# Performance work log

Measured on AMD Instinct MI355X. Metric: run time of the kernel, lower is better.

## Reference

```python
import jax, jax.numpy as jnp
import numpy as np

NEG_INIT = -1.0e9  # matches torch.full(..., -1000000000.0)

def setup_inputs() -> dict:
    key = jax.random.key(0)
    ks = jax.random.split(key, 12)
    N, B, F, C = 4_000_000, 16384, 3, 4
    flat_muons = jax.random.normal(ks[0], (N, F), dtype=jnp.float32)
    batch_index = jnp.sort(jax.random.randint(ks[1], (N,), 0, B))
    conditions = jax.random.normal(ks[2], (B, C), dtype=jnp.float32)
    def lin(k, fin, fout):
        k1, k2 = jax.random.split(k)
        bound = 1.0 / np.sqrt(fin)
        W = jax.random.uniform(k1, (fin, fout), jnp.float32, -bound, bound)
        b = jax.random.uniform(k2, (fout,), jnp.float32, -bound, bound)
        return W, b
    W1, b1 = lin(ks[3], F + C, 64)
    W2, b2 = lin(ks[4], 64, 128)
    W3, b3 = lin(ks[5], 128 + C, 128)
    W4, b4 = lin(ks[6], 128, 1)
    return {"flat_muons": flat_muons, "batch_index": batch_index,
            "conditions": conditions, "batch_size": B,
            "W1": W1, "b1": b1, "W2": W2, "b2": b2,
            "W3": W3, "b3": b3, "W4": W4, "b4": b4}

def reference(flat_muons, batch_index, conditions, batch_size,
              W1, b1, W2, b2, W3, b3, W4, b4):
    lrelu = lambda x: jax.nn.leaky_relu(x, 0.2)
    flat_cond = conditions[batch_index]                       # [N, C] gather
    point_in = jnp.concatenate([flat_muons, flat_cond], axis=1)
    h = lrelu(point_in @ W1 + b1)                             # [N, 64]
    point_feats = lrelu(h @ W2 + b2)                          # [N, 128]
    # segmented amax with -1e9 baseline (scatter_reduce_ amax semantics)
    global_feats = jnp.full((batch_size, 128), NEG_INIT, dtype=point_feats.dtype)
    global_feats = global_feats.at[batch_index].max(point_feats)
    decision_in = jnp.concatenate([global_feats, conditions], axis=1)
    score = lrelu(decision_in @ W3 + b3) @ W4 + b4            # [B, 1]
    return score
```

## Files before the change

### kernel.cpp

```cpp
#include <hip/hip_runtime.h>

typedef float f32x4 __attribute__((ext_vector_type(4)));
typedef float f32x16 __attribute__((ext_vector_type(16)));
typedef _Float16 half8 __attribute__((ext_vector_type(8)));
typedef _Float16 half2v __attribute__((ext_vector_type(2)));
typedef unsigned u32x4 __attribute__((ext_vector_type(4)));

__device__ __forceinline__ unsigned f2mono(float f) {
  unsigned u = __float_as_uint(f);
  return (u & 0x80000000u) ? ~u : (u | 0x80000000u);
}
__device__ __forceinline__ float mono2f(unsigned u) {
  return (u & 0x80000000u) ? __uint_as_float(u & 0x7fffffffu) : __uint_as_float(~u);
}
__device__ __forceinline__ float lrelu(float x) { return fmaxf(x, 0.2f * x); }
__device__ __forceinline__ unsigned pkrtz(float a, float b) {
  return __builtin_bit_cast(unsigned, __builtin_amdgcn_cvt_pkrtz(a, b));
}
__device__ __forceinline__ unsigned lrelu_pk(float a, float b) {
  const half2v v = __builtin_bit_cast(half2v, pkrtz(a, b));
  const half2v s = v * (half2v){(_Float16)0.2f, (_Float16)0.2f};
  return __builtin_bit_cast(unsigned, __builtin_elementwise_max(v, s));
}
__device__ __forceinline__ half8 ash8(u32x4 u) { return __builtin_bit_cast(half8, u); }
__device__ __forceinline__ float max16(const f32x16& a) {
  const float m1 = fmaxf(fmaxf(a[0], a[1]), a[2]);
  const float m2 = fmaxf(fmaxf(a[3], a[4]), a[5]);
  const float m3 = fmaxf(fmaxf(a[6], a[7]), a[8]);
  const float m4 = fmaxf(fmaxf(a[9], a[10]), a[11]);
  const float m5 = fmaxf(fmaxf(a[12], a[13]), a[14]);
  return fmaxf(fmaxf(fmaxf(m1, m2), m3), fmaxf(fmaxf(m4, m5), a[15]));
}
__device__ __forceinline__ void plswap(unsigned& x, unsigned& y) {
  asm volatile("v_permlane32_swap_b32 %0, %1" : "+v"(x), "+v"(y));
}
__device__ __forceinline__ float xhalf_max(float m) {
  unsigned a = __float_as_uint(m), b = a;
  plswap(a, b);
  return fmaxf(__uint_as_float(a), __uint_as_float(b));
}

__global__ void sc_init(unsigned* __restrict__ gf, int total4) {
  int i = blockIdx.x * blockDim.x + threadIdx.x;
  if (i < total4) {
    unsigned m = f2mono(-1.0e9f);
    ((uint4*)gf)[i] = make_uint4(m, m, m, m);
  }
}

__global__ __launch_bounds__(256, 2) void sc_main(
    const float* __restrict__ muons, const int* __restrict__ bidx,
    const float* __restrict__ cond, const float* __restrict__ W1,
    const float* __restrict__ b1, const float* __restrict__ W2,
    const float* __restrict__ b2, unsigned* __restrict__ gf, int N, int CPW) {
  __shared__ __align__(16) _Float16 w2f[8192];
  __shared__ __align__(16) _Float16 w1e[1024];

  const int t = threadIdx.x;
  const int w = t >> 6;
  const int lane = t & 63;
  const int col = lane & 31;
  const int kh2 = lane >> 5;

  {
    const int j = t & 127, kh = t >> 7;
    for (int kk = 0; kk < 32; ++kk) {
      const int k = kh * 32 + kk;
      w2f[((k >> 3) * 128 + j) * 8 + (k & 7)] = (_Float16)W2[k * 128 + j];
    }
  }
  if (t < 128) {
    const int j = t & 63, kc = t >> 6;
    for (int e = 0; e < 8; ++e) {
      const int kp = kc * 8 + e;
      float val;
      if (kp < 7)       val = W1[kp * 64 + j];
      else if (kp < 14) val = W1[(kp - 7) * 64 + j];
      else if (kp == 14) val = b1[j];
      else { const float b = b1[j]; val = b - (float)(_Float16)b; }
      w1e[(kc * 64 + j) * 8 + e] = (_Float16)val;
    }
  }
  __syncthreads();

  float b2v[4];
  #pragma unroll
  for (int jt = 0; jt < 4; ++jt) b2v[jt] = b2[jt * 32 + col];
  f32x16 zf;
  #pragma unroll
  for (int e = 0; e < 16; ++e) zf[e] = 0.0f;

  const int gwave = blockIdx.x * 4 + w;
  const int start = gwave * CPW;
  if (start >= N) return;
  const int end = min(start + CPW, N);
  const int prevb = (start == 0) ? -1 : bidx[start - 1];
  const int nextb = (end >= N) ? -1 : bidx[end];
  int run_b = bidx[start];
  float run_s[4];
  #pragma unroll
  for (int jt = 0; jt < 4; ++jt) run_s[jt] = -3.0e38f;

  const half8 a1lo = *(const half8*)&w1e[(kh2 * 64 + col) * 8];
  const half8 a1hi = *(const half8*)&w1e[(kh2 * 64 + 32 + col) * 8];

  auto FLUSH = [&](int b, const float* m) {
    const bool interior = (b != prevb) && (b != nextb);
    if (lane < 32) {
      #pragma unroll
      for (int jt = 0; jt < 4; ++jt) {
        if (m[jt] > -2.9e38f) {
          const unsigned enc = f2mono(lrelu(m[jt] + b2v[jt]));
          unsigned* addr = &gf[b * 128 + jt * 32 + col];
          if (interior) *addr = enc; else atomicMax(addr, enc);
        }
      }
    }
  };

  auto DECOMP = [&](float mu0, float mu1, float mu2, const f32x4& c4) -> half8 {
    float in[7];
    in[0] = mu0; in[1] = mu1; in[2] = mu2;
    in[3] = c4.x; in[4] = c4.y; in[5] = c4.z; in[6] = c4.w;
    const unsigned pA0 = pkrtz(in[0], in[1]);
    const unsigned pA1 = pkrtz(in[2], in[3]);
    const unsigned pA2 = pkrtz(in[4], in[5]);
    const half2v hA0 = __builtin_bit_cast(half2v, pA0);
    const half2v hA1 = __builtin_bit_cast(half2v, pA1);
    const half2v hA2 = __builtin_bit_cast(half2v, pA2);
    const float xl0 = in[0] - (float)hA0[0];
    const unsigned pA3 = pkrtz(in[6], xl0);
    const half2v hA3 = __builtin_bit_cast(half2v, pA3);
    const unsigned pB0 = pkrtz(in[1] - (float)hA0[1], in[2] - (float)hA1[0]);
    const unsigned pB1 = pkrtz(in[3] - (float)hA1[1], in[4] - (float)hA2[0]);
    const unsigned pB2 = pkrtz(in[5] - (float)hA2[1], in[6] - (float)hA3[0]);
    const unsigned pB3 = 0x3C003C00u;
    u32x4 bu;
    bu[0] = kh2 ? pB0 : pA0;
    bu[1] = kh2 ? pB1 : pA1;
    bu[2] = kh2 ? pB2 : pA2;
    bu[3] = kh2 ? pB3 : pA3;
    return ash8(bu);
  };

  auto MKAFRAG = [&](const f32x16& a0, const f32x16& a1, half8* Afr) {
    unsigned pk0[8], pk1[8];
    #pragma unroll
    for (int q = 0; q < 4; ++q) {
      pk0[2 * q]     = lrelu_pk(a0[4 * q],     a0[4 * q + 1]);
      pk0[2 * q + 1] = lrelu_pk(a0[4 * q + 2], a0[4 * q + 3]);
      pk1[2 * q]     = lrelu_pk(a1[4 * q],     a1[4 * q + 1]);
      pk1[2 * q + 1] = lrelu_pk(a1[4 * q + 2], a1[4 * q + 3]);
    }
    #pragma unroll
    for (int ks = 0; ks < 4; ++ks) {
      const unsigned* s = (ks < 2) ? pk0 : pk1;
      const int base = (ks & 1) * 4;
      unsigned x0 = s[base + 0], y0 = s[base + 2];
      unsigned x1 = s[base + 1], y1 = s[base + 3];
      plswap(x0, y0);
      plswap(x1, y1);
      u32x4 au;
      au[0] = x0; au[1] = x1; au[2] = y0; au[3] = y1;
      Afr[ks] = ash8(au);
    }
  };

  auto L2SEG = [&](const half8* Afr, int bi) {
    f32x16 acc2[4];
    #pragma unroll
    for (int ks = 0; ks < 4; ++ks) {
      const int kcb = (2 * ks + kh2) * 128;
      #pragma unroll
      for (int jt = 0; jt < 4; ++jt) {
        const half8 B = *(const half8*)&w2f[(kcb + jt * 32 + col) * 8];
        acc2[jt] = __builtin_amdgcn_mfma_f32_32x32x16_f16(Afr[ks], B,
                                                          (ks == 0) ? zf : acc2[jt], 0, 0, 0);
      }
    }
    const int bA = __shfl(bi, 0);
    const int bB = __shfl(bi, 31);
    if (bA != run_b) {
      FLUSH(run_b, run_s);
      #pragma unroll
      for (int jt = 0; jt < 4; ++jt) run_s[jt] = -3.0e38f;
      run_b = bA;
    }
    if (bA == bB) {
      #pragma unroll
      for (int jt = 0; jt < 4; ++jt)
        run_s[jt] = fmaxf(run_s[jt], xhalf_max(max16(acc2[jt])));
    } else {
      int pbi[16];
      #pragma unroll
      for (int r = 0; r < 16; ++r) {
        const int rr = (r & 3) + ((r >> 2) << 3) + (kh2 << 2);
        pbi[r] = __shfl(bi, rr);
      }
      for (int b = bA; b <= bB; ++b) {
        float m[4];
        #pragma unroll
        for (int jt = 0; jt < 4; ++jt) {
          float mm = -3.0e38f;
          #pragma unroll
          for (int r = 0; r < 16; ++r)
            if (pbi[r] == b) mm = fmaxf(mm, acc2[jt][r]);
          mm = xhalf_max(mm);
          if (b == bA) mm = fmaxf(mm, run_s[jt]);
          m[jt] = mm;
        }
        if (b < bB) {
          FLUSH(b, m);
        } else {
          #pragma unroll
          for (int jt = 0; jt < 4; ++jt) run_s[jt] = m[jt];
        }
      }
      run_b = bB;
    }
  };

  int pA = min(start + col, N - 1);
  int pB = min(start + 32 + col, N - 1);
  int biA_n = bidx[pA], biB_n = bidx[pB];
  float muA_n[3] = {muons[pA * 3], muons[pA * 3 + 1], muons[pA * 3 + 2]};
  float muB_n[3] = {muons[pB * 3], muons[pB * 3 + 1], muons[pB * 3 + 2]};
  f32x4 c4A_n = *(const f32x4*)&cond[biA_n * 4];
  f32x4 c4B_n = *(const f32x4*)&cond[biB_n * 4];

  for (int pbase = start; pbase < end; pbase += 64) {
    const int biA = biA_n, biB = biB_n;
    const float mA0 = muA_n[0], mA1 = muA_n[1], mA2 = muA_n[2];
    const float mB0 = muB_n[0], mB1 = muB_n[1], mB2 = muB_n[2];
    const f32x4 c4A = c4A_n, c4B = c4B_n;

    const int pnA = min(pbase + 64 + col, N - 1);
    const int pnB = min(pbase + 96 + col, N - 1);
    biA_n = bidx[pnA]; biB_n = bidx[pnB];
    muA_n[0] = muons[pnA * 3]; muA_n[1] = muons[pnA * 3 + 1]; muA_n[2] = muons[pnA * 3 + 2];
    muB_n[0] = muons[pnB * 3]; muB_n[1] = muons[pnB * 3 + 1]; muB_n[2] = muons[pnB * 3 + 2];

    const half8 bfrA = DECOMP(mA0, mA1, mA2, c4A);
    const half8 bfrB = DECOMP(mB0, mB1, mB2, c4B);
    const f32x16 aA0 = __builtin_amdgcn_mfma_f32_32x32x16_f16(a1lo, bfrA, zf, 0, 0, 0);
    const f32x16 aA1 = __builtin_amdgcn_mfma_f32_32x32x16_f16(a1hi, bfrA, zf, 0, 0, 0);
    const f32x16 aB0 = __builtin_amdgcn_mfma_f32_32x32x16_f16(a1lo, bfrB, zf, 0, 0, 0);
    const f32x16 aB1 = __builtin_amdgcn_mfma_f32_32x32x16_f16(a1hi, bfrB, zf, 0, 0, 0);

    c4A_n = *(const f32x4*)&cond[biA_n * 4];
    c4B_n = *(const f32x4*)&cond[biB_n * 4];

    half8 AfrA[4], AfrB[4];
    MKAFRAG(aA0, aA1, AfrA);
    MKAFRAG(aB0, aB1, AfrB);

    L2SEG(AfrA, biA);
    L2SEG(AfrB, biB);
  }
  FLUSH(run_b, run_s);
}

__global__ __launch_bounds__(128) void sc_final(
    const unsigned* __restrict__ gf, const float* __restrict__ cond,
    const float* __restrict__ W3, const float* __restrict__ b3,
    const float* __restrict__ W4, const float* __restrict__ b4,
    float* __restrict__ out, int B) {
  __shared__ __align__(16) float w3t[128 * 132];
  __shared__ float b3s[128], w4s[128];
  __shared__ __align__(16) float din[8 * 132];
  __shared__ float wred[16];
  const int t = threadIdx.x;
  for (int k = 0; k < 132; ++k) w3t[t * 132 + k] = W3[k * 128 + t];
  b3s[t] = b3[t];
  w4s[t] = W4[t];
  __syncthreads();

  const int nocts = (B + 7) >> 3;
  for (int oc = blockIdx.x; oc < nocts; oc += gridDim.x) {
    const int rbase = oc << 3;
    #pragma unroll
    for (int r = 0; r < 8; ++r) {
      const int row = rbase + r;
      if (row < B) {
        din[r * 132 + t] = mono2f(gf[row * 128 + t]);
        if (t < 4) din[r * 132 + 128 + t] = cond[row * 4 + t];
      }
    }
    __syncthreads();
    float a8[8];
    #pragma unroll
    for (int r = 0; r < 8; ++r) a8[r] = b3s[t];
    for (int kg = 0; kg < 33; ++kg) {
      const f32x4 wv = *(const f32x4*)&w3t[t * 132 + kg * 4];
      #pragma unroll
      for (int r = 0; r < 8; ++r) {
        const f32x4 dv = *(const f32x4*)&din[r * 132 + kg * 4];
        a8[r] += wv[0] * dv[0] + wv[1] * dv[1] + wv[2] * dv[2] + wv[3] * dv[3];
      }
    }
    const float w4v = w4s[t];
    #pragma unroll
    for (int r = 0; r < 8; ++r) a8[r] = lrelu(a8[r]) * w4v;
    const int lane = t & 63;
    const int wv_ = t >> 6;
    #pragma unroll
    for (int r = 0; r < 8; ++r) {
      float s = a8[r];
      s += __shfl_xor(s, 1);  s += __shfl_xor(s, 2);
      s += __shfl_xor(s, 4);  s += __shfl_xor(s, 8);
      s += __shfl_xor(s, 16); s += __shfl_xor(s, 32);
      if (lane == 0) wred[wv_ * 8 + r] = s;
    }
    __syncthreads();
    if (t < 8) {
      const int row = rbase + t;
      if (row < B) out[row] = wred[t] + wred[8 + t] + b4[0];
    }
    __syncthreads();
  }
}

extern "C" void kernel_launch(void* const* d_in, const int* in_sizes, int n_in,
                              void* d_out, int out_size, void* d_ws, size_t ws_size,
                              hipStream_t stream) {
  const float* muons = (const float*)d_in[0];
  const int* bidx = (const int*)d_in[1];
  const float* cond = (const float*)d_in[2];
  const float* W1 = (const float*)d_in[4];
  const float* b1 = (const float*)d_in[5];
  const float* W2 = (const float*)d_in[6];
  const float* b2 = (const float*)d_in[7];
  const float* W3 = (const float*)d_in[8];
  const float* b3 = (const float*)d_in[9];
  const float* W4 = (const float*)d_in[10];
  const float* b4 = (const float*)d_in[11];
  float* out = (float*)d_out;
  const int N = in_sizes[1];
  const int B = out_size;
  unsigned* gf = (unsigned*)d_ws;

  const int total4 = (B * 128) / 4;
  sc_init<<<(total4 + 255) / 256, 256, 0, stream>>>(gf, total4);

  const int nblocks = 2048;
  const int nwaves = nblocks * 4;
  const int cpw = (((N + nwaves - 1) / nwaves) + 63) & ~63;
  sc_main<<<nblocks, 256, 0, stream>>>(muons, bidx, cond, W1, b1, W2, b2, gf, N, cpw);
  sc_final<<<1024, 128, 0, stream>>>(gf, cond, W3, b3, W4, b4, out, B);
  (void)n_in; (void)ws_size;
}
```

Baseline: 151.4 us.

## Use split-fp16 MFMA for final MLP and add fast two-segment flush path

The final decision MLP, previously scalar fp32 FMAs over LDS-staged rows, now runs on 32x32x16 fp16 MFMA. W3 and the inputs are each split into high and low fp16 parts to keep near-fp32 accuracy, and the bias is folded in as an extra input column set to 1. Each wave handles 32 rows, and the launch shrinks to just enough blocks for B. In the main kernel, the cross-half max reduction moves into FLUSH so it runs only when a segment is written. A ballot/popcount fast path handles tiles that span exactly two segments without per-row shuffles. The split-precision product costs three MFMAs per tile, and each block now rebuilds a larger fp16 copy of W3 in LDS.

```diff
diff --git a/kernel.cpp b/kernel.cpp
--- a/kernel.cpp
+++ b/kernel.cpp
@@ -106,11 +106,14 @@
 
   auto FLUSH = [&](int b, const float* m) {
     const bool interior = (b != prevb) && (b != nextb);
+    float mm[4];
+    #pragma unroll
+    for (int jt = 0; jt < 4; ++jt) mm[jt] = xhalf_max(m[jt]);
     if (lane < 32) {
       #pragma unroll
       for (int jt = 0; jt < 4; ++jt) {
-        if (m[jt] > -2.9e38f) {
-          const unsigned enc = f2mono(lrelu(m[jt] + b2v[jt]));
+        if (mm[jt] > -2.9e38f) {
+          const unsigned enc = f2mono(lrelu(mm[jt] + b2v[jt]));
           unsigned* addr = &gf[b * 128 + jt * 32 + col];
           if (interior) *addr = enc; else atomicMax(addr, enc);
         }
@@ -189,34 +192,59 @@
     if (bA == bB) {
       #pragma unroll
       for (int jt = 0; jt < 4; ++jt)
-        run_s[jt] = fmaxf(run_s[jt], xhalf_max(max16(acc2[jt])));
+        run_s[jt] = fmaxf(run_s[jt], max16(acc2[jt]));
     } else {
-      int pbi[16];
-      #pragma unroll
-      for (int r = 0; r < 16; ++r) {
-        const int rr = (r & 3) + ((r >> 2) << 3) + (kh2 << 2);
-        pbi[r] = __shfl(bi, rr);
+      const unsigned long long ball = __ballot(bi == bA);
+      const int split = (int)__popcll(ball & 0xffffffffULL);
+      const int bS = __shfl(bi, split);
+      if (bS == bB) {
+        float mA[4], mB[4];
+        #pragma unroll
+        for (int jt = 0; jt < 4; ++jt) { mA[jt] = -3.0e38f; mB[jt] = -3.0e38f; }
+        #pragma unroll
+        for (int r = 0; r < 16; ++r) {
+          const int rr = (r & 3) + ((r >> 2) << 3) + (kh2 << 2);
+          const bool inA = rr < split;
+          #pragma unroll
+          for (int jt = 0; jt < 4; ++jt) {
+            const float v = acc2[jt][r];
+            mA[jt] = fmaxf(mA[jt], inA ? v : -3.0e38f);
+            mB[jt] = fmaxf(mB[jt], inA ? -3.0e38f : v);
+          }
+        }
+        #pragma unroll
+        for (int jt = 0; jt < 4; ++jt) mA[jt] = fmaxf(mA[jt], run_s[jt]);
+        FLUSH(bA, mA);
+        #pragma unroll
+        for (int jt = 0; jt < 4; ++jt) run_s[jt] = mB[jt];
+        run_b = bB;
+      } else {
+        int pbi[16];
+        #pragma unroll
+        for (int r = 0; r < 16; ++r) {
+          const int rr = (r & 3) + ((r >> 2) << 3) + (kh2 << 2);
+          pbi[r] = __shfl(bi, rr);
+        }
+        for (int b = bA; b <= bB; ++b) {
+          float m[4];
+          #pragma unroll
+          for (int jt = 0; jt < 4; ++jt) {
+            float mm = -3.0e38f;
+            #pragma unroll
+            for (int r = 0; r < 16; ++r)
+              if (pbi[r] == b) mm = fmaxf(mm, acc2[jt][r]);
+            if (b == bA) mm = fmaxf(mm, run_s[jt]);
+            m[jt] = mm;
+          }
+          if (b < bB) {
+            FLUSH(b, m);
+          } else {
+            #pragma unroll
+            for (int jt = 0; jt < 4; ++jt) run_s[jt] = m[jt];
+          }
+        }
+        run_b = bB;
       }
-      for (int b = bA; b <= bB; ++b) {
-        float m[4];
-        #pragma unroll
-        for (int jt = 0; jt < 4; ++jt) {
-          float mm = -3.0e38f;
-          #pragma unroll
-          for (int r = 0; r < 16; ++r)
-            if (pbi[r] == b) mm = fmaxf(mm, acc2[jt][r]);
-          mm = xhalf_max(mm);
-          if (b == bA) mm = fmaxf(mm, run_s[jt]);
-          m[jt] = mm;
-        }
-        if (b < bB) {
-          FLUSH(b, m);
-        } else {
-          #pragma unroll
-          for (int jt = 0; jt < 4; ++jt) run_s[jt] = m[jt];
-        }
-      }
-      run_b = bB;
     }
   };
 
@@ -260,64 +288,96 @@
   FLUSH(run_b, run_s);
 }
 
-__global__ __launch_bounds__(128) void sc_final(
+__global__ __launch_bounds__(256, 2) void sc_final(
     const unsigned* __restrict__ gf, const float* __restrict__ cond,
     const float* __restrict__ W3, const float* __restrict__ b3,
     const float* __restrict__ W4, const float* __restrict__ b4,
     float* __restrict__ out, int B) {
-  __shared__ __align__(16) float w3t[128 * 132];
-  __shared__ float b3s[128], w4s[128];
-  __shared__ __align__(16) float din[8 * 132];
-  __shared__ float wred[16];
+  __shared__ __align__(16) _Float16 w3h[18432];
+  __shared__ __align__(16) _Float16 w3l[18432];
+  __shared__ float w4s[128];
   const int t = threadIdx.x;
-  for (int k = 0; k < 132; ++k) w3t[t * 132 + k] = W3[k * 128 + t];
-  b3s[t] = b3[t];
-  w4s[t] = W4[t];
+  const int w = t >> 6, lane = t & 63, col = lane & 31, kh2 = lane >> 5;
+
+  for (int i = t; i < 144 * 128; i += 256) {
+    const int k = i >> 7, j = i & 127;
+    float v = 0.0f;
+    if (k < 132) v = W3[k * 128 + j];
+    else if (k == 132) v = b3[j];
+    const _Float16 h = (_Float16)v;
+    const int a = ((k >> 3) * 128 + j) * 8 + (k & 7);
+    w3h[a] = h;
+    w3l[a] = (_Float16)(v - (float)h);
+  }
+  if (t < 128) w4s[t] = W4[t];
   __syncthreads();
 
-  const int nocts = (B + 7) >> 3;
-  for (int oc = blockIdx.x; oc < nocts; oc += gridDim.x) {
-    const int rbase = oc << 3;
-    #pragma unroll
-    for (int r = 0; r < 8; ++r) {
-      const int row = rbase + r;
-      if (row < B) {
-        din[r * 132 + t] = mono2f(gf[row * 128 + t]);
-        if (t < 4) din[r * 132 + 128 + t] = cond[row * 4 + t];
-      }
-    }
-    __syncthreads();
-    float a8[8];
-    #pragma unroll
-    for (int r = 0; r < 8; ++r) a8[r] = b3s[t];
-    for (int kg = 0; kg < 33; ++kg) {
-      const f32x4 wv = *(const f32x4*)&w3t[t * 132 + kg * 4];
+  const int tile = blockIdx.x * 4 + w;
+  const int row = tile * 32 + col;
+  const int rc = min(row, B - 1);
+
+  uint4 g[16];
+  #pragma unroll
+  for (int kc = 0; kc < 8; ++kc) {
+    const int base = rc * 128 + kc * 16 + kh2 * 8;
+    g[2 * kc]     = *(const uint4*)&gf[base];
+    g[2 * kc + 1] = *(const uint4*)&gf[base + 4];
+  }
+  const f32x4 c4 = *(const f32x4*)&cond[rc * 4];
+
+  f32x16 zf;
+  #pragma unroll
+  for (int e = 0; e < 16; ++e) zf[e] = 0.0f;
+  f32x16 acc[4];
+
+  #pragma unroll
+  for (int kc = 0; kc < 9; ++kc) {
+    float v[8];
+    if (kc < 8) {
+      const uint4 ga = g[2 * kc], gb = g[2 * kc + 1];
+      v[0] = mono2f(ga.x); v[1] = mono2f(ga.y); v[2] = mono2f(ga.z); v[3] = mono2f(ga.w);
+      v[4] = mono2f(gb.x); v[5] = mono2f(gb.y); v[6] = mono2f(gb.z); v[7] = mono2f(gb.w);
+    } else if (kh2 == 0) {
+      v[0] = c4.x; v[1] = c4.y; v[2] = c4.z; v[3] = c4.w;
+      v[4] = 1.0f; v[5] = 0.0f; v[6] = 0.0f; v[7] = 0.0f;
+    } else {
       #pragma unroll
-      for (int r = 0; r < 8; ++r) {
-        const f32x4 dv = *(const f32x4*)&din[r * 132 + kg * 4];
-        a8[r] += wv[0] * dv[0] + wv[1] * dv[1] + wv[2] * dv[2] + wv[3] * dv[3];
-      }
-    }
-    const float w4v = w4s[t];
-    #pragma unroll
-    for (int r = 0; r < 8; ++r) a8[r] = lrelu(a8[r]) * w4v;
-    const int lane = t & 63;
-    const int wv_ = t >> 6;
-    #pragma unroll
-    for (int r = 0; r < 8; ++r) {
-      float s = a8[r];
-      s += __shfl_xor(s, 1);  s += __shfl_xor(s, 2);
-      s += __shfl_xor(s, 4);  s += __shfl_xor(s, 8);
-      s += __shfl_xor(s, 16); s += __shfl_xor(s, 32);
-      if (lane == 0) wred[wv_ * 8 + r] = s;
-    }
-    __syncthreads();
-    if (t < 8) {
-      const int row = rbase + t;
-      if (row < B) out[row] = wred[t] + wred[8 + t] + b4[0];
-    }
-    __syncthreads();
-  }
+      for (int e = 0; e < 8; ++e) v[e] = 0.0f;
+    }
+    u32x4 bh, bl;
+    #pragma unroll
+    for (int q = 0; q < 4; ++q) {
+      const unsigned ph = pkrtz(v[2 * q], v[2 * q + 1]);
+      const half2v hh = __builtin_bit_cast(half2v, ph);
+      bh[q] = ph;
+      bl[q] = pkrtz(v[2 * q] - (float)hh[0], v[2 * q + 1] - (float)hh[1]);
+    }
+    const half8 Bh = ash8(bh), Bl = ash8(bl);
+    #pragma unroll
+    for (int jt = 0; jt < 4; ++jt) {
+      const int a = ((kc * 2 + kh2) * 128 + jt * 32 + col) * 8;
+      const half8 Ah = *(const half8*)&w3h[a];
+      const half8 Al = *(const half8*)&w3l[a];
+      f32x16 c = (kc == 0) ? zf : acc[jt];
+      c = __builtin_amdgcn_mfma_f32_32x32x16_f16(Ah, Bh, c, 0, 0, 0);
+      c = __builtin_amdgcn_mfma_f32_32x32x16_f16(Ah, Bl, c, 0, 0, 0);
+      c = __builtin_amdgcn_mfma_f32_32x32x16_f16(Al, Bh, c, 0, 0, 0);
+      acc[jt] = c;
+    }
+  }
+
+  float partial = 0.0f;
+  #pragma unroll
+  for (int jt = 0; jt < 4; ++jt)
+    #pragma unroll
+    for (int r = 0; r < 16; ++r) {
+      const int j = jt * 32 + (r & 3) + ((r >> 2) << 3) + (kh2 << 2);
+      partial += lrelu(acc[jt][r]) * w4s[j];
+    }
+  unsigned pa = __float_as_uint(partial), pb = pa;
+  plswap(pa, pb);
+  const float tot = __uint_as_float(pa) + __uint_as_float(pb);
+  if (lane < 32 && row < B) out[row] = tot + b4[0];
 }
 
 extern "C" void kernel_launch(void* const* d_in, const int* in_sizes, int n_in,
@@ -346,6 +406,9 @@
   const int nwaves = nblocks * 4;
   const int cpw = (((N + nwaves - 1) / nwaves) + 63) & ~63;
   sc_main<<<nblocks, 256, 0, stream>>>(muons, bidx, cond, W1, b1, W2, b2, gf, N, cpw);
-  sc_final<<<1024, 128, 0, stream>>>(gf, cond, W3, b3, W4, b4, out, B);
+
+  const int ftiles = (B + 31) / 32;
+  const int fblocks = (ftiles + 3) / 4;
+  sc_final<<<fblocks, 256, 0, stream>>>(gf, cond, W3, b3, W4, b4, out, B);
   (void)n_in; (void)ws_size;
 }
```

Measured after the change: 124.2 us. 1.22x faster.
